# Optimization experiments

Measured on AMD Instinct MI355X. Metric: run time of the kernel, lower is better.

Reference implementation:

```python
import jax, jax.numpy as jnp
import numpy as np

B, T, HID = 4, 2048, 1024
NH = 16
HS = HID // NH  # 64


def setup_inputs() -> dict:
    key = jax.random.key(0)
    ks = jax.random.split(key, 9)
    s = 1.0 / np.sqrt(HID)
    return {
        "x": jax.random.normal(ks[0], (B, T, HID), dtype=jnp.float32),
        "Wq": jax.random.uniform(ks[1], (HID, HID), jnp.float32, -s, s),
        "bq": jax.random.uniform(ks[2], (HID,), jnp.float32, -s, s),
        "Wk": jax.random.uniform(ks[3], (HID, HID), jnp.float32, -s, s),
        "bk": jax.random.uniform(ks[4], (HID,), jnp.float32, -s, s),
        "Wv": jax.random.uniform(ks[5], (HID, HS), jnp.float32, -s, s),
        "bv": jax.random.uniform(ks[6], (HS,), jnp.float32, -s, s),
        "Wo": jax.random.uniform(ks[7], (HS, HID), jnp.float32, -1.0 / np.sqrt(HS), 1.0 / np.sqrt(HS)),
        "bo": jax.random.uniform(ks[8], (HID,), jnp.float32, -1.0 / np.sqrt(HS), 1.0 / np.sqrt(HS)),
    }


def reference(x, Wq, bq, Wk, bk, Wv, bv, Wo, bo):
    scale = HS ** -0.5
    q = (x @ Wq + bq).reshape(B, T, NH, HS)  # (B,T,H,hs)
    k = (x @ Wk + bk).reshape(B, T, NH, HS)
    v = x @ Wv + bv                          # shared V: (B,T,hs)
    # scores: (B,H,T,T)
    scores = jnp.einsum("bqhd,bkhd->bhqk", q, k) * scale
    attn = jax.nn.softmax(scores, axis=-1)
    attn_avg = attn.mean(axis=1)             # (B,T,T), head-averaged
    out = jnp.einsum("bqk,bkd->bqd", attn_avg, v) @ Wo + bo  # (B,T,HID)
    return out, attn_avg
```

## Files before the change

### kernel.cpp

```cpp
#include <hip/hip_runtime.h>
#include <math.h>

#define Bc   4
#define Tt   2048
#define HIDc 1024
#define NHc  16
#define HSc  64
#define BTc  (Bc * Tt)
#define SCALE 0.125f

typedef __attribute__((ext_vector_type(8))) short bf16x8;
typedef __attribute__((ext_vector_type(4))) float f32x4;

__device__ __forceinline__ unsigned short f2bf(float f) {
    unsigned u = __float_as_uint(f);
    u = u + 0x7FFFu + ((u >> 16) & 1u);
    return (unsigned short)(u >> 16);
}

__global__ __launch_bounds__(256) void gemm_f32(
    const float* __restrict__ A, const float* __restrict__ Bm,
    const float* __restrict__ bias, float* __restrict__ C,
    int M, int N, int K, long sA, long sB, long sC)
{
    A  += (long)blockIdx.z * sA;
    Bm += (long)blockIdx.z * sB;
    C  += (long)blockIdx.z * sC;

    __shared__ float As[16][64];
    __shared__ float Bs[16][64];

    const int tid  = threadIdx.x;
    const int tx   = tid & 15;
    const int ty   = tid >> 4;
    const int row0 = blockIdx.y * 64;
    const int col0 = blockIdx.x * 64;

    const int la_r = tid >> 2;
    const int la_c = (tid & 3) << 2;
    const int lb_r = tid >> 4;
    const int lb_c = (tid & 15) << 2;

    float acc[4][4] = {};

    for (int k0 = 0; k0 < K; k0 += 16) {
        float4 av = *(const float4*)&A[(long)(row0 + la_r) * K + k0 + la_c];
        float4 bv = *(const float4*)&Bm[(long)(k0 + lb_r) * N + col0 + lb_c];
        __syncthreads();
        As[la_c + 0][la_r] = av.x;
        As[la_c + 1][la_r] = av.y;
        As[la_c + 2][la_r] = av.z;
        As[la_c + 3][la_r] = av.w;
        *(float4*)&Bs[lb_r][lb_c] = bv;
        __syncthreads();
#pragma unroll
        for (int kk = 0; kk < 16; ++kk) {
            float4 a = *(float4*)&As[kk][ty << 2];
            float4 b = *(float4*)&Bs[kk][tx << 2];
            float ar[4] = {a.x, a.y, a.z, a.w};
            float br[4] = {b.x, b.y, b.z, b.w};
#pragma unroll
            for (int i = 0; i < 4; ++i)
#pragma unroll
                for (int j = 0; j < 4; ++j)
                    acc[i][j] = fmaf(ar[i], br[j], acc[i][j]);
        }
    }

    float4 bvv = make_float4(0.f, 0.f, 0.f, 0.f);
    if (bias) bvv = *(const float4*)&bias[col0 + (tx << 2)];
#pragma unroll
    for (int i = 0; i < 4; ++i) {
        int m = row0 + (ty << 2) + i;
        float4 o;
        o.x = acc[i][0] + bvv.x;
        o.y = acc[i][1] + bvv.y;
        o.z = acc[i][2] + bvv.z;
        o.w = acc[i][3] + bvv.w;
        *(float4*)&C[(long)m * N + col0 + (tx << 2)] = o;
    }
}

__global__ __launch_bounds__(256) void gemm_skinny_splitk(
    const float* __restrict__ A, const float* __restrict__ Bm,
    float* __restrict__ C, int K, int KC, long sA, long sB, long sC)
{
    A  += (long)blockIdx.z * sA;
    Bm += (long)blockIdx.z * sB;
    C  += (long)blockIdx.z * sC;

    __shared__ float As[16][64];
    __shared__ float Bs[16][64];

    const int tid  = threadIdx.x;
    const int tx   = tid & 15;
    const int ty   = tid >> 4;
    const int row0 = blockIdx.x * 64;
    const int kbeg = blockIdx.y * KC;

    const int la_r = tid >> 2;
    const int la_c = (tid & 3) << 2;
    const int lb_r = tid >> 4;
    const int lb_c = (tid & 15) << 2;

    float acc[4][4] = {};

    for (int k0 = kbeg; k0 < kbeg + KC; k0 += 16) {
        float4 av = *(const float4*)&A[(long)(row0 + la_r) * K + k0 + la_c];
        float4 bv = *(const float4*)&Bm[(long)(k0 + lb_r) * 64 + lb_c];
        __syncthreads();
        As[la_c + 0][la_r] = av.x;
        As[la_c + 1][la_r] = av.y;
        As[la_c + 2][la_r] = av.z;
        As[la_c + 3][la_r] = av.w;
        *(float4*)&Bs[lb_r][lb_c] = bv;
        __syncthreads();
#pragma unroll
        for (int kk = 0; kk < 16; ++kk) {
            float4 a = *(float4*)&As[kk][ty << 2];
            float4 b = *(float4*)&Bs[kk][tx << 2];
            float ar[4] = {a.x, a.y, a.z, a.w};
            float br[4] = {b.x, b.y, b.z, b.w};
#pragma unroll
            for (int i = 0; i < 4; ++i)
#pragma unroll
                for (int j = 0; j < 4; ++j)
                    acc[i][j] = fmaf(ar[i], br[j], acc[i][j]);
        }
    }

#pragma unroll
    for (int i = 0; i < 4; ++i) {
        const int m = row0 + (ty << 2) + i;
#pragma unroll
        for (int j = 0; j < 4; ++j)
            atomicAdd(&C[(long)m * 64 + (tx << 2) + j], acc[i][j]);
    }
}

__global__ __launch_bounds__(256) void init_bias64(
    float* __restrict__ C, const float* __restrict__ bias, long n)
{
    long idx = (long)blockIdx.x * 256 + threadIdx.x;
    if (idx < n) C[idx] = bias ? bias[idx & 63] : 0.f;
}

__global__ __launch_bounds__(256) void cast_bf16(
    const float* __restrict__ src, unsigned short* __restrict__ dst, long n)
{
    long i = ((long)blockIdx.x * 256 + threadIdx.x) * 4;
    if (i >= n) return;
    float4 v = *(const float4*)&src[i];
    ushort4 o;
    o.x = f2bf(v.x); o.y = f2bf(v.y); o.z = f2bf(v.z); o.w = f2bf(v.w);
    *(ushort4*)&dst[i] = o;
}

__global__ __launch_bounds__(256) void transpose_cast(
    const float* __restrict__ W, unsigned short* __restrict__ Wt)
{
    __shared__ float t[32][33];
    const int k0 = blockIdx.x * 32, n0 = blockIdx.y * 32;
    const int c = threadIdx.x & 31, r = threadIdx.x >> 5;
#pragma unroll
    for (int rr = r; rr < 32; rr += 8)
        t[rr][c] = W[(long)(k0 + rr) * HIDc + n0 + c];
    __syncthreads();
#pragma unroll
    for (int rr = r; rr < 32; rr += 8)
        Wt[(long)(n0 + rr) * HIDc + k0 + c] = f2bf(t[c][rr]);
}

__global__ __launch_bounds__(256) void gemm_bt_bf16(
    const unsigned short* __restrict__ A, const unsigned short* __restrict__ Bt,
    const float* __restrict__ bias, unsigned short* __restrict__ C,
    int M, int N, int K)
{
    __shared__ unsigned short As[128][72];
    __shared__ unsigned short Bs[128][72];

    const int tid  = threadIdx.x;
    const int row0 = blockIdx.y * 128;
    const int col0 = blockIdx.x * 128;
    const int w  = tid >> 6, L = tid & 63;
    const int wm = (w & 1) * 64, wn = (w >> 1) * 64;
    const int lr = tid >> 3;
    const int lc = (tid & 7) * 8;
    const int ml = L & 15, q8 = (L >> 4) * 8, q4 = (L >> 4) * 4;

    f32x4 acc[4][4];
#pragma unroll
    for (int i = 0; i < 4; ++i)
#pragma unroll
        for (int j = 0; j < 4; ++j)
            acc[i][j] = (f32x4){0.f, 0.f, 0.f, 0.f};

    for (int k0 = 0; k0 < K; k0 += 64) {
        __syncthreads();
#pragma unroll
        for (int rr = 0; rr < 128; rr += 32) {
            *(float4*)&As[lr + rr][lc] = *(const float4*)&A[(long)(row0 + lr + rr) * K + k0 + lc];
            *(float4*)&Bs[lr + rr][lc] = *(const float4*)&Bt[(long)(col0 + lr + rr) * K + k0 + lc];
        }
        __syncthreads();
#pragma unroll
        for (int kk = 0; kk < 64; kk += 32) {
            bf16x8 a[4], b[4];
#pragma unroll
            for (int i = 0; i < 4; ++i) a[i] = *(bf16x8*)&As[wm + i * 16 + ml][kk + q8];
#pragma unroll
            for (int j = 0; j < 4; ++j) b[j] = *(bf16x8*)&Bs[wn + j * 16 + ml][kk + q8];
#pragma unroll
            for (int i = 0; i < 4; ++i)
#pragma unroll
                for (int j = 0; j < 4; ++j)
                    acc[i][j] = __builtin_amdgcn_mfma_f32_16x16x32_bf16(a[i], b[j], acc[i][j], 0, 0, 0);
        }
    }

#pragma unroll
    for (int j = 0; j < 4; ++j) {
        const int col = col0 + wn + j * 16 + ml;
        const float bj = bias ? bias[col] : 0.f;
#pragma unroll
        for (int i = 0; i < 4; ++i) {
#pragma unroll
            for (int r = 0; r < 4; ++r) {
                const int row = row0 + wm + i * 16 + q4 + r;
                C[(long)row * N + col] = f2bf(acc[i][j][r] + bj);
            }
        }
    }
}

__global__ __launch_bounds__(256) void attn_denom(
    const unsigned short* __restrict__ qb, const unsigned short* __restrict__ kb,
    float* __restrict__ linv)
{
    const int qt = blockIdx.x, h = blockIdx.y, b = blockIdx.z;
    __shared__ unsigned short Qs[64][72];
    __shared__ unsigned short Ks[64][72];
    __shared__ float lsum[64];

    const int tid = threadIdx.x;
    const int L = tid & 63, w = tid >> 6;
    const int rw = (w >> 1) * 32, kh = (w & 1) * 32;
    const int sr = tid >> 2, sc = (tid & 3) * 16;
    const int ml = L & 15, q8 = (L >> 4) * 8, q4 = (L >> 4) * 4;

    {
        const unsigned short* s = qb + ((long)(b * Tt + qt * 64 + sr) * HIDc + h * HSc + sc);
        *(float4*)&Qs[sr][sc]     = *(const float4*)s;
        *(float4*)&Qs[sr][sc + 8] = *(const float4*)(s + 8);
    }
    if (tid < 64) lsum[tid] = 0.f;

    float lacc[2][4] = {};

    for (int kt = 0; kt < Tt / 64; ++kt) {
        const unsigned short* s = kb + ((long)(b * Tt + kt * 64 + sr) * HIDc + h * HSc + sc);
        float4 v0 = *(const float4*)s;
        float4 v1 = *(const float4*)(s + 8);
        __syncthreads();
        *(float4*)&Ks[sr][sc]     = v0;
        *(float4*)&Ks[sr][sc + 8] = v1;
        __syncthreads();

        f32x4 acc[2][2];
#pragma unroll
        for (int i = 0; i < 2; ++i)
#pragma unroll
            for (int j = 0; j < 2; ++j) acc[i][j] = (f32x4){0.f, 0.f, 0.f, 0.f};
#pragma unroll
        for (int kk = 0; kk < 64; kk += 32) {
            bf16x8 a0 = *(bf16x8*)&Qs[rw + ml][kk + q8];
            bf16x8 a1 = *(bf16x8*)&Qs[rw + 16 + ml][kk + q8];
            bf16x8 b0 = *(bf16x8*)&Ks[kh + ml][kk + q8];
            bf16x8 b1 = *(bf16x8*)&Ks[kh + 16 + ml][kk + q8];
            acc[0][0] = __builtin_amdgcn_mfma_f32_16x16x32_bf16(a0, b0, acc[0][0], 0, 0, 0);
            acc[0][1] = __builtin_amdgcn_mfma_f32_16x16x32_bf16(a0, b1, acc[0][1], 0, 0, 0);
            acc[1][0] = __builtin_amdgcn_mfma_f32_16x16x32_bf16(a1, b0, acc[1][0], 0, 0, 0);
            acc[1][1] = __builtin_amdgcn_mfma_f32_16x16x32_bf16(a1, b1, acc[1][1], 0, 0, 0);
        }
#pragma unroll
        for (int i = 0; i < 2; ++i)
#pragma unroll
            for (int j = 0; j < 2; ++j)
#pragma unroll
                for (int r = 0; r < 4; ++r)
                    lacc[i][r] += __expf(acc[i][j][r] * SCALE);
    }

#pragma unroll
    for (int i = 0; i < 2; ++i)
#pragma unroll
        for (int r = 0; r < 4; ++r) {
            float v = lacc[i][r];
            v += __shfl_xor(v, 1, 16);
            v += __shfl_xor(v, 2, 16);
            v += __shfl_xor(v, 4, 16);
            v += __shfl_xor(v, 8, 16);
            if (ml == 0) atomicAdd(&lsum[rw + i * 16 + q4 + r], v);
        }
    __syncthreads();
    if (tid < 64)
        linv[((long)(b * NHc + h)) * Tt + qt * 64 + tid] = 1.0f / (lsum[tid] * (float)NHc);
}

__global__ __launch_bounds__(256) void attn_avg_w(
    const unsigned short* __restrict__ qb, const unsigned short* __restrict__ kb,
    const float* __restrict__ linv, float* __restrict__ attn)
{
    const int kt = blockIdx.x, qt = blockIdx.y, b = blockIdx.z;
    __shared__ unsigned short Qs[64][72];
    __shared__ unsigned short Ks[64][72];
    __shared__ float invs[64];

    const int tid = threadIdx.x;
    const int L = tid & 63, w = tid >> 6;
    const int rw = (w >> 1) * 32, kh = (w & 1) * 32;
    const int sr = tid >> 2, sc = (tid & 3) * 16;
    const int ml = L & 15, q8 = (L >> 4) * 8, q4 = (L >> 4) * 4;

    float pacc[2][2][4] = {};

    for (int h = 0; h < NHc; ++h) {
        const unsigned short* sq = qb + ((long)(b * Tt + qt * 64 + sr) * HIDc + h * HSc + sc);
        const unsigned short* sk = kb + ((long)(b * Tt + kt * 64 + sr) * HIDc + h * HSc + sc);
        float4 q0 = *(const float4*)sq;
        float4 q1 = *(const float4*)(sq + 8);
        float4 k0 = *(const float4*)sk;
        float4 k1 = *(const float4*)(sk + 8);
        float iv = 0.f;
        if (tid < 64) iv = linv[((long)(b * NHc + h)) * Tt + qt * 64 + tid];
        __syncthreads();
        *(float4*)&Qs[sr][sc]     = q0;
        *(float4*)&Qs[sr][sc + 8] = q1;
        *(float4*)&Ks[sr][sc]     = k0;
        *(float4*)&Ks[sr][sc + 8] = k1;
        if (tid < 64) invs[tid] = iv;
        __syncthreads();

        f32x4 acc[2][2];
#pragma unroll
        for (int i = 0; i < 2; ++i)
#pragma unroll
            for (int j = 0; j < 2; ++j) acc[i][j] = (f32x4){0.f, 0.f, 0.f, 0.f};
#pragma unroll
        for (int kk = 0; kk < 64; kk += 32) {
            bf16x8 a0 = *(bf16x8*)&Qs[rw + ml][kk + q8];
            bf16x8 a1 = *(bf16x8*)&Qs[rw + 16 + ml][kk + q8];
            bf16x8 b0 = *(bf16x8*)&Ks[kh + ml][kk + q8];
            bf16x8 b1 = *(bf16x8*)&Ks[kh + 16 + ml][kk + q8];
            acc[0][0] = __builtin_amdgcn_mfma_f32_16x16x32_bf16(a0, b0, acc[0][0], 0, 0, 0);
            acc[0][1] = __builtin_amdgcn_mfma_f32_16x16x32_bf16(a0, b1, acc[0][1], 0, 0, 0);
            acc[1][0] = __builtin_amdgcn_mfma_f32_16x16x32_bf16(a1, b0, acc[1][0], 0, 0, 0);
            acc[1][1] = __builtin_amdgcn_mfma_f32_16x16x32_bf16(a1, b1, acc[1][1], 0, 0, 0);
        }
#pragma unroll
        for (int i = 0; i < 2; ++i)
#pragma unroll
            for (int r = 0; r < 4; ++r) {
                const float iv_r = invs[rw + i * 16 + q4 + r];
#pragma unroll
                for (int j = 0; j < 2; ++j)
                    pacc[i][j][r] += __expf(acc[i][j][r] * SCALE) * iv_r;
            }
    }

#pragma unroll
    for (int i = 0; i < 2; ++i)
#pragma unroll
        for (int j = 0; j < 2; ++j)
#pragma unroll
            for (int r = 0; r < 4; ++r) {
                const long row = b * Tt + qt * 64 + rw + i * 16 + q4 + r;
                const int  col = kt * 64 + kh + j * 16 + ml;
                attn[row * Tt + col] = pacc[i][j][r];
            }
}

extern "C" void kernel_launch(void* const* d_in, const int* in_sizes, int n_in,
                              void* d_out, int out_size, void* d_ws, size_t ws_size,
                              hipStream_t stream)
{
    const float* x  = (const float*)d_in[0];
    const float* Wq = (const float*)d_in[1];
    const float* bq = (const float*)d_in[2];
    const float* Wk = (const float*)d_in[3];
    const float* bk = (const float*)d_in[4];
    const float* Wv = (const float*)d_in[5];
    const float* bv = (const float*)d_in[6];
    const float* Wo = (const float*)d_in[7];
    const float* bo = (const float*)d_in[8];

    float* out  = (float*)d_out;
    float* attn = out + (long)BTc * HIDc;

    unsigned short* xb  = (unsigned short*)d_ws;
    unsigned short* Wqt = xb  + (long)BTc * HIDc;
    unsigned short* Wkt = Wqt + (long)HIDc * HIDc;
    unsigned short* qb  = Wkt + (long)HIDc * HIDc;
    unsigned short* kb  = qb  + (long)BTc * HIDc;
    float* v    = (float*)(kb + (long)BTc * HIDc);
    float* linv = v    + (long)BTc * HSc;
    float* o1   = linv + (long)Bc * NHc * Tt;

    dim3 blk(256);

    cast_bf16<<<dim3((BTc * HIDc) / 1024), blk, 0, stream>>>(x, xb, (long)BTc * HIDc);
    transpose_cast<<<dim3(32, 32), blk, 0, stream>>>(Wq, Wqt);
    transpose_cast<<<dim3(32, 32), blk, 0, stream>>>(Wk, Wkt);
    init_bias64<<<dim3((BTc * HSc) / 256), blk, 0, stream>>>(v,  bv,      (long)BTc * HSc);
    init_bias64<<<dim3((BTc * HSc) / 256), blk, 0, stream>>>(o1, nullptr, (long)BTc * HSc);

    gemm_bt_bf16<<<dim3(HIDc / 128, BTc / 128), blk, 0, stream>>>(xb, Wqt, bq, qb, BTc, HIDc, HIDc);
    gemm_bt_bf16<<<dim3(HIDc / 128, BTc / 128), blk, 0, stream>>>(xb, Wkt, bk, kb, BTc, HIDc, HIDc);

    gemm_skinny_splitk<<<dim3(BTc / 64, HIDc / 128, 1), blk, 0, stream>>>(
        x, Wv, v, HIDc, 128, 0, 0, 0);

    attn_denom<<<dim3(Tt / 64, NHc, Bc), blk, 0, stream>>>(qb, kb, linv);

    attn_avg_w<<<dim3(Tt / 64, Tt / 64, Bc), blk, 0, stream>>>(qb, kb, linv, attn);

    gemm_skinny_splitk<<<dim3(Tt / 64, Tt / 256, Bc), blk, 0, stream>>>(
        attn, v, o1, Tt, 256, (long)Tt * Tt, (long)Tt * HSc, (long)Tt * HSc);

    gemm_f32<<<dim3(HIDc / 64, BTc / 64, 1), blk, 0, stream>>>(o1, Wo, bo, out, BTc, HIDc, HSc, 0, 0, 0);
}
```

Measured before the change: 499.6 us.

## Fuse attn_avg @ V into the attention-average kernel with atomic accumulation

The head-averaged attention tile is converted to bf16 in shared memory and multiplied by a bf16-transposed V tile with MFMA inside attn_avg_w. Partial results are atomically added into o1, which removes the separate split-K GEMM that re-read the full attention matrix (B*T*T floats). The cost is extra LDS use, a bf16 rounding of P and V, and many float atomics, 64 k-tiles per output element, which also makes the summation order nondeterministic.

```diff
diff --git a/kernel.cpp b/kernel.cpp
--- a/kernel.cpp
+++ b/kernel.cpp
@@ -309,11 +309,14 @@
 
 __global__ __launch_bounds__(256) void attn_avg_w(
     const unsigned short* __restrict__ qb, const unsigned short* __restrict__ kb,
-    const float* __restrict__ linv, float* __restrict__ attn)
+    const float* __restrict__ linv, const float* __restrict__ v,
+    float* __restrict__ attn, float* __restrict__ o1)
 {
     const int kt = blockIdx.x, qt = blockIdx.y, b = blockIdx.z;
     __shared__ unsigned short Qs[64][72];
     __shared__ unsigned short Ks[64][72];
+    __shared__ unsigned short Ps[64][72];
+    __shared__ unsigned short Vst[64][72];
     __shared__ float invs[64];
 
     const int tid = threadIdx.x;
@@ -321,6 +324,12 @@
     const int rw = (w >> 1) * 32, kh = (w & 1) * 32;
     const int sr = tid >> 2, sc = (tid & 3) * 16;
     const int ml = L & 15, q8 = (L >> 4) * 8, q4 = (L >> 4) * 4;
+
+#pragma unroll
+    for (int e = tid; e < 4096; e += 256) {
+        const int r = e >> 6, d = e & 63;
+        Vst[d][r] = f2bf(v[((long)(b * Tt + kt * 64 + r)) * 64 + d]);
+    }
 
     float pacc[2][2][4] = {};
 
@@ -374,9 +383,39 @@
         for (int j = 0; j < 2; ++j)
 #pragma unroll
             for (int r = 0; r < 4; ++r) {
-                const long row = b * Tt + qt * 64 + rw + i * 16 + q4 + r;
-                const int  col = kt * 64 + kh + j * 16 + ml;
-                attn[row * Tt + col] = pacc[i][j][r];
+                const int qrow = rw + i * 16 + q4 + r;
+                const int kcol = kh + j * 16 + ml;
+                attn[((long)(b * Tt + qt * 64 + qrow)) * Tt + kt * 64 + kcol] = pacc[i][j][r];
+                Ps[qrow][kcol] = f2bf(pacc[i][j][r]);
+            }
+    __syncthreads();
+
+    const int qh = rw, dh = kh;
+    f32x4 uacc[2][2];
+#pragma unroll
+    for (int i = 0; i < 2; ++i)
+#pragma unroll
+        for (int j = 0; j < 2; ++j) uacc[i][j] = (f32x4){0.f, 0.f, 0.f, 0.f};
+#pragma unroll
+    for (int kk = 0; kk < 64; kk += 32) {
+        bf16x8 a0 = *(bf16x8*)&Ps[qh + ml][kk + q8];
+        bf16x8 a1 = *(bf16x8*)&Ps[qh + 16 + ml][kk + q8];
+        bf16x8 b0 = *(bf16x8*)&Vst[dh + ml][kk + q8];
+        bf16x8 b1 = *(bf16x8*)&Vst[dh + 16 + ml][kk + q8];
+        uacc[0][0] = __builtin_amdgcn_mfma_f32_16x16x32_bf16(a0, b0, uacc[0][0], 0, 0, 0);
+        uacc[0][1] = __builtin_amdgcn_mfma_f32_16x16x32_bf16(a0, b1, uacc[0][1], 0, 0, 0);
+        uacc[1][0] = __builtin_amdgcn_mfma_f32_16x16x32_bf16(a1, b0, uacc[1][0], 0, 0, 0);
+        uacc[1][1] = __builtin_amdgcn_mfma_f32_16x16x32_bf16(a1, b1, uacc[1][1], 0, 0, 0);
+    }
+#pragma unroll
+    for (int i = 0; i < 2; ++i)
+#pragma unroll
+        for (int j = 0; j < 2; ++j)
+#pragma unroll
+            for (int r = 0; r < 4; ++r) {
+                const long row = (long)(b * Tt + qt * 64 + qh + i * 16 + q4 + r);
+                const int  d   = dh + j * 16 + ml;
+                atomicAdd(&o1[row * 64 + d], uacc[i][j][r]);
             }
 }
 
@@ -422,10 +461,7 @@
 
     attn_denom<<<dim3(Tt / 64, NHc, Bc), blk, 0, stream>>>(qb, kb, linv);
 
-    attn_avg_w<<<dim3(Tt / 64, Tt / 64, Bc), blk, 0, stream>>>(qb, kb, linv, attn);
-
-    gemm_skinny_splitk<<<dim3(Tt / 64, Tt / 256, Bc), blk, 0, stream>>>(
-        attn, v, o1, Tt, 256, (long)Tt * Tt, (long)Tt * HSc, (long)Tt * HSc);
+    attn_avg_w<<<dim3(Tt / 64, Tt / 64, Bc), blk, 0, stream>>>(qb, kb, linv, v, attn, o1);
 
     gemm_f32<<<dim3(HIDc / 64, BTc / 64, 1), blk, 0, stream>>>(o1, Wo, bo, out, BTc, HIDc, HSc, 0, 0, 0);
 }
```

After: 451.3 us. 1.11x faster.
